# Performance work log

Measured on AMD Instinct MI355X. Metric: run time of the kernel, lower is better.

The kernel has to match this reference:

```python
import jax, jax.numpy as jnp
from jax import lax
import numpy as np

H = W = 224
N = H * W
T = 25          # landscape sample points
K_MAX = 2       # number of landscapes
M_PTS = 64      # max persistence-diagram points kept (top persistence)
OUT_F = 50
CHUNK = 512     # pixels per DTM chunk


def _make_offsets(m0):
    # static, sorted-by-distance local window covering >= m0 fraction of mass for near-uniform weights
    r = int(np.ceil(np.sqrt(m0 * N / np.pi) * 1.3))
    dy, dx = np.meshgrid(np.arange(-r, r + 1), np.arange(-r, r + 1), indexing="ij")
    d2 = (dy * dy + dx * dx).astype(np.float32).ravel()
    o = np.argsort(d2, kind="stable")
    return jnp.asarray(dy.ravel()[o]), jnp.asarray(dx.ravel()[o]), jnp.asarray(d2[o]), r

_OFF = {m0: _make_offsets(m0) for m0 in (0.05, 0.2)}


def _dtm(w_img, m0):
    """Weighted distance-to-measure on the unit-spacing 224x224 grid.
    dtm(x)^2 = (1/(m0*W)) * sum of w_j * d_j^2 over nearest grid points until cumulative
    weight reaches m0*W (partial weight on the crossing point). Offsets are pre-sorted by
    distance (identical for every pixel), so no per-pixel sort is needed."""
    dy, dx, d2, r = _OFF[m0]
    B = w_img.shape[0]
    wp = jnp.pad(w_img, ((0, 0), (r, r), (r, r)))
    thr = m0 * w_img.sum(axis=(1, 2))                      # (B,)
    pix = jnp.arange(N).reshape(N // CHUNK, CHUNK)

    def body(p):
        y = p // W + r
        x = p % W + r
        vals = wp[:, y[:, None] + dy[None, :], x[:, None] + dx[None, :]]  # (B,C,O)
        c = jnp.cumsum(vals, axis=-1)
        used = jnp.minimum(jnp.maximum(thr[:, None, None] - (c - vals), 0.0), vals)
        return jnp.einsum("bco,o->bc", used, d2) / thr[:, None]

    dtm2 = lax.map(jax.checkpoint(body), pix)              # (n_chunks, B, CHUNK)
    return jnp.sqrt(jnp.maximum(dtm2.transpose(1, 0, 2).reshape(B, N), 0.0))


def _h0_pairs_np(f_batch):
    """0-dim persistent homology (sublevel filtration, 4-connectivity) via union-find.
    Returns indices of birth/death pixels so birth/death VALUES can be gathered
    differentiably in jax (PLLay-style gradients)."""
    f_batch = np.asarray(f_batch)
    B = f_batch.shape[0]
    b_idx = np.zeros((B, M_PTS), np.int32)
    d_idx = np.zeros((B, M_PTS), np.int32)
    mask = np.zeros((B, M_PTS), np.bool_)
    for bb in range(B):
        f = f_batch[bb]
        order = np.argsort(f, kind="stable")
        parent = np.full(N, -1, np.int64)
        pairs = []
        for i in order:
            i = int(i)
            parent[i] = i
            y, x = divmod(i, W)
            nbs = []
            if y > 0: nbs.append(i - W)
            if y < H - 1: nbs.append(i + W)
            if x > 0: nbs.append(i - 1)
            if x < W - 1: nbs.append(i + 1)
            for nb in nbs:
                if parent[nb] < 0:
                    continue
                ri = i
                while parent[ri] != ri:
                    parent[ri] = parent[parent[ri]]; ri = parent[ri]
                rn = nb
                while parent[rn] != rn:
                    parent[rn] = parent[parent[rn]]; rn = parent[rn]
                if ri == rn:
                    continue
                if f[ri] <= f[rn]:
                    elder, young = ri, rn
                else:
                    elder, young = rn, ri
                pairs.append((young, i))   # elder rule: younger component dies here
                parent[young] = elder
        pairs.append((int(np.argmin(f)), int(np.argmax(f))))  # essential class
        pa = np.asarray(pairs, np.int64)
        pers = f[pa[:, 1]] - f[pa[:, 0]]
        keep = np.argsort(-pers)[:M_PTS]
        k = len(keep)
        b_idx[bb, :k] = pa[keep, 0]
        d_idx[bb, :k] = pa[keep, 1]
        mask[bb, :k] = pers[keep] > 0
    return b_idx, d_idx, mask


def _topo_layer(x_img, m0, tseq, gw, gb):
    # AdTopoLayer: DTM -> H0 persistence diagram -> persistence landscapes at tseq -> Linear
    dt = _dtm(x_img, m0)                                   # (B, N)
    B = dt.shape[0]
    shapes = (jax.ShapeDtypeStruct((B, M_PTS), np.int32),
              jax.ShapeDtypeStruct((B, M_PTS), np.int32),
              jax.ShapeDtypeStruct((B, M_PTS), np.bool_))
    b_idx, d_idx, mask = jax.pure_callback(_h0_pairs_np, shapes, lax.stop_gradient(dt))
    birth = jnp.take_along_axis(dt, b_idx, axis=1)         # differentiable gather
    death = jnp.take_along_axis(dt, d_idx, axis=1)
    death = jnp.where(mask, death, birth)                  # invalid slots -> zero tent
    t = tseq[None, None, :]                                # (1,1,T)
    tents = jnp.maximum(jnp.minimum(t - birth[:, :, None], death[:, :, None] - t), 0.0)
    lam, _ = lax.top_k(tents.transpose(0, 2, 1), K_MAX)    # (B,T,K): k-th largest tents
    feat = lam.transpose(0, 2, 1).reshape(B, K_MAX * T)    # (B,50)
    return feat @ gw.T + gb


def _forward(input, params):
    xs = []
    for m0, g in ((0.05, "1"), (0.2, "2")):
        for c in range(3):
            n = "t" + g + str(c + 1)
            xs.append(_topo_layer(input[:, c], m0, params[n + "_tseq"], params[n + "_w"], params[n + "_b"]))
    x = jnp.concatenate(xs, axis=-1)                       # (B, 300)
    signal = jnp.abs(lax.stop_gradient(x)).sum(axis=0)     # (300,) detached signal
    output = jax.nn.relu(x) @ params["fc_w"].T + params["fc_b"]
    return output, signal


def setup_inputs():
    key = jax.random.key(0)
    ks = jax.random.split(key, 8)
    B = 2
    inp = {"input": jax.random.uniform(ks[0], (B, 3, H, W), jnp.float32)}
    centers = {"1": 20.0, "2": 40.0}   # typical DTM value ranges for m0=0.05 / 0.2
    i = 1
    for g in ("1", "2"):
        for c in ("1", "2", "3"):
            n = "t" + g + c
            kk = jax.random.fold_in(ks[1], i)
            inp[n + "_tseq"] = jnp.linspace(centers[g] - 15.0, centers[g] + 15.0, T).astype(jnp.float32)
            inp[n + "_w"] = 0.1 * jax.random.normal(kk, (OUT_F, K_MAX * T), jnp.float32)
            inp[n + "_b"] = jnp.zeros((OUT_F,), jnp.float32)
            i += 1
    inp["fc_w"] = 0.1 * jax.random.normal(ks[2], (7, 6 * OUT_F), jnp.float32)
    inp["fc_b"] = jnp.zeros((7,), jnp.float32)
    return inp


def reference(input, t11_tseq, t11_w, t11_b, t12_tseq, t12_w, t12_b, t13_tseq, t13_w, t13_b, t21_tseq, t21_w, t21_b, t22_tseq, t22_w, t22_b, t23_tseq, t23_w, t23_b, fc_w, fc_b):
    params = dict(t11_tseq=t11_tseq, t11_w=t11_w, t11_b=t11_b,
                  t12_tseq=t12_tseq, t12_w=t12_w, t12_b=t12_b,
                  t13_tseq=t13_tseq, t13_w=t13_w, t13_b=t13_b,
                  t21_tseq=t21_tseq, t21_w=t21_w, t21_b=t21_b,
                  t22_tseq=t22_tseq, t22_w=t22_w, t22_b=t22_b,
                  t23_tseq=t23_tseq, t23_w=t23_w, t23_b=t23_b,
                  fc_w=fc_w, fc_b=fc_b)
    return _forward(input, params)
```

## Files before the change

### kernel.cpp

```cpp
#include <hip/hip_runtime.h>
#include <stdint.h>

#define HWDIM 224
#define NPIX (HWDIM*HWDIM)
#define NFIELD 12
#define TT 25

#define R1v 37
#define PW1v (HWDIM + 2*R1v)
#define C1v  (PW1v + 1)
#define R2v 74
#define PW2v (HWDIM + 2*R2v)
#define C2v  (PW2v + 1)

#define HSIZE 16384
#define FCAP 4096
#define RHASH 4096
#define DON 36

typedef unsigned long long u64;

struct LayerParams {
    const float* tseq[6];
    const float* gw[6];
    const float* gb[6];
};

constexpr size_t alup(size_t x) { return (x + 255) & ~(size_t)255; }
constexpr size_t SZPA = (size_t)6*PW1v*C1v*4;
constexpr size_t SZPB = (size_t)6*PW2v*C2v*4;
constexpr size_t OFF_SUMS = 0;
constexpr size_t OFF_P0A = alup(OFF_SUMS + 8*4);
constexpr size_t OFF_PZA = alup(OFF_P0A + SZPA);
constexpr size_t OFF_P0B = alup(OFF_PZA + 2*SZPA);
constexpr size_t OFF_PZB = alup(OFF_P0B + SZPB);
constexpr size_t OFF_DT   = alup(OFF_PZB + 2*SZPB);
constexpr size_t OFF_KEY  = alup(OFF_DT   + (size_t)NFIELD*NPIX*4);
constexpr size_t OFF_HP   = alup(OFF_KEY  + (size_t)NFIELD*NPIX*8);
constexpr size_t OFF_HB   = alup(OFF_HP   + (size_t)NFIELD*HSIZE*8);
constexpr size_t OFF_X    = alup(OFF_HB   + (size_t)NFIELD*HSIZE*8);


__global__ __launch_bounds__(1024) void k_sums(const float* __restrict__ inp, float* __restrict__ sums) {
    int img = blockIdx.x;
    const float* p = inp + (size_t)img * NPIX;
    __shared__ float red[1024];
    float s = 0.f;
    for (int i = threadIdx.x; i < NPIX; i += 1024) s += p[i];
    red[threadIdx.x] = s; __syncthreads();
    for (int w = 512; w > 0; w >>= 1) {
        if (threadIdx.x < w) red[threadIdx.x] += red[threadIdx.x + w];
        __syncthreads();
    }
    if (threadIdx.x == 0) sums[img] = red[0];
}

__global__ __launch_bounds__(64) void k_prefix(const float* __restrict__ inp,
        float* __restrict__ p0a, float2* __restrict__ pza,
        float* __restrict__ p0b, float2* __restrict__ pzb) {
    int bidx = blockIdx.x;
    const int tot0 = 6 * PW1v;
    int g = (bidx >= tot0);
    int rem = g ? (bidx - tot0) : bidx;
    const int PW = g ? PW2v : PW1v, R = g ? R2v : R1v, C = PW + 1;
    int img = rem / PW, row = rem % PW;
    float* P0 = (g ? p0b : p0a) + ((size_t)img*PW + row) * C;
    float2* PZ = (g ? pzb : pza) + ((size_t)img*PW + row) * C;
    int iy = row - R;
    bool rowok = ((unsigned)iy < HWDIM);
    const float* src = inp + (size_t)img*NPIX + (size_t)(rowok ? iy : 0)*HWDIM;
    const int lane = threadIdx.x;
    if (lane == 0) { P0[0] = 0.f; PZ[0] = make_float2(0.f, 0.f); }
    float c0 = 0.f, c1 = 0.f, c2 = 0.f;
    for (int i = 0; i < 6; ++i) {
        int k = i*64 + lane;
        float v = 0.f;
        if (k < PW && rowok) { int ix = k - R; if ((unsigned)ix < HWDIM) v = src[ix]; }
        float xd = (float)k;
        float w0 = v, w1 = v*xd, w2 = v*xd*xd;
        #pragma unroll
        for (int off = 1; off < 64; off <<= 1) {
            float t0 = __shfl_up(w0, off), t1 = __shfl_up(w1, off), t2 = __shfl_up(w2, off);
            if (lane >= off) { w0 += t0; w1 += t1; w2 += t2; }
        }
        if (k < PW) {
            P0[k+1] = c0 + w0;
            PZ[k+1] = make_float2(c1 + w1, c2 + w2);
        }
        c0 += __shfl(w0, 63); c1 += __shfl(w1, 63); c2 += __shfl(w2, 63);
    }
}

__device__ __forceinline__ int k_init_exact(int X, int R) {
    int K = (int)sqrtf((float)X) + 1;
    if (K > R) K = R;
    while (K > 0 && K*K > X) --K;
    return K;
}

__device__ __forceinline__ float dmass1(int X, const float* __restrict__ P0, int bidx,
        int C, int R) {
    float m = 0.f;
    int K = 0;
    if (X >= 0) {
        K = k_init_exact(X, R);
        m = P0[bidx+K+1] - P0[bidx-K];
    }
    int t = X - 1, step = 3;
    const float* __restrict__ Pu = P0 - C;
    const float* __restrict__ Pd = P0 + C;
    for (int dyy = 1; dyy <= R; ++dyy) {
        if (__all(t < 0)) break;
        if (t >= 0) {
            while (K*K > t) --K;
            int A = bidx + K + 1, B = bidx - K;
            m += (Pu[A] - Pu[B]) + (Pd[A] - Pd[B]);
        }
        t -= step; step += 2; Pu -= C; Pd += C;
    }
    return m;
}

__global__ __launch_bounds__(256) void k_dtm(const float* __restrict__ sums,
        const float* __restrict__ p0a, const float2* __restrict__ pza,
        const float* __restrict__ p0b, const float2* __restrict__ pzb,
        float* __restrict__ dt, u64* __restrict__ key) {
    const int xcd = blockIdx.x & 7, slot = blockIdx.x >> 3;
    int f, blk;
    if (xcd < 6) {
        if (slot < 196)            { f = 6 + xcd; blk = slot; }
        else if (slot < 196 + DON) { f = xcd; blk = (196 - DON) + (slot - 196); }
        else return;
    } else {
        const int per = 196 - DON;
        if (slot >= 3*per) return;
        int q = slot / per;
        f = (xcd - 6)*3 + q; blk = slot - q*per;
    }
    const int layer = f >> 1, b = f & 1;
    const int g = layer / 3, c = layer % 3;
    const int img = b*3 + c;
    const int R = g ? R2v : R1v, PW = g ? PW2v : PW1v, C = PW + 1;
    const int R2 = 2*R*R;
    const float thr = (g ? 0.2f : 0.05f) * sums[img];
    const float* __restrict__ P0 = (g ? p0b : p0a) + (size_t)img*PW*C;
    const float2* __restrict__ PZ = (g ? pzb : pza) + (size_t)img*PW*C;

    const int p = blk*256 + threadIdx.x;
    const int y = p / HWDIM, x = p % HWDIM;
    const int xc = x + R;
    const int bidx = (y + R)*C + xc;

    const int NP = g ? 7 : 6;
    const int WSTOP = g ? 86 : 43;
    int lo = 0, hi = R2 + 1;
    for (int it = 0; it < NP; ++it) {
        int X = (lo + hi) >> 1;
        float m = dmass1(X, P0, bidx, C, R);
        if (m >= thr) hi = X; else lo = X + 1;
    }
    for (int rit = 0; rit < 14; ++rit) {
        bool act = (hi == R2 + 1) ? (lo < hi) : (hi - lo > WSTOP);
        if (__all(!act)) break;
        int X = act ? ((lo + hi) >> 1) : -1;
        float m = dmass1(X, P0, bidx, C, R);
        if (X >= 0) { if (m >= thr) hi = X; else lo = X + 1; }
    }
    const bool nr = (hi == R2 + 1);
    const int  Dst = nr ? lo : ((lo + hi) >> 1);
    const bool cross = nr ? (lo <= R2) : true;
    const int  Xin = cross ? (Dst - 1) : R2;

    float m_in = 0.f, ws = 0.f;
    const float c2n = -2.f * (float)xc;
    const int xc2i = xc * xc;
    int K = 0;
    if (Xin >= 0) {
        K = k_init_exact(Xin, R);
        int A = bidx+K+1, B = bidx-K;
        float s0 = P0[A] - P0[B]; float2 zA = PZ[A], zB = PZ[B];
        m_in += s0; ws += fmaf((float)xc2i, s0, fmaf(c2n, zA.x - zB.x, zA.y - zB.y));
    }
    {
        int t = Xin - 1, step = 3, d2 = 1;
        const float* __restrict__ Pu = P0 - C;
        const float* __restrict__ Pd = P0 + C;
        const float2* __restrict__ Zu = PZ - C;
        const float2* __restrict__ Zd = PZ + C;
        for (int dyy = 1; dyy <= R; ++dyy) {
            if (__all(t < 0)) break;
            if (t >= 0) {
                while (K*K > t) --K;
                int A = bidx+K+1, B = bidx-K;
                float c1 = (float)(d2 + xc2i);
                { float s0 = Pu[A]-Pu[B]; float2 zA = Zu[A], zB = Zu[B];
                  m_in += s0; ws += fmaf(c1, s0, fmaf(c2n, zA.x - zB.x, zA.y - zB.y)); }
                { float s0 = Pd[A]-Pd[B]; float2 zA = Zd[A], zB = Zd[B];
                  m_in += s0; ws += fmaf(c1, s0, fmaf(c2n, zA.x - zB.x, zA.y - zB.y)); }
            }
            t -= step; d2 += step; step += 2;
            Pu -= C; Pd += C; Zu -= C; Zd += C;
        }
    }
    float s = cross ? (ws + (float)Dst * (thr - m_in)) : ws;
    float d = sqrtf(fmaxf(s / thr, 0.f));
    dt[(size_t)f*NPIX + p] = d;
    key[(size_t)f*NPIX + p] = ((u64)__float_as_uint(d) << 32) | (unsigned)p;
}

__device__ inline unsigned hash64(u64 x) {
    x ^= x >> 33; x *= 0xff51afd7ed558ccdULL;
    x ^= x >> 33; x *= 0xc4ceb9fe1a85ec53ULL;
    x ^= x >> 33;
    return (unsigned)x;
}

struct FinSh {
    u64 ek[FCAP];
    unsigned int epk[FCAP];
    unsigned int eab[FCAP];
    unsigned short eru[FCAP];
    int rhk[RHASH];
    short ufp[RHASH];
    float rdt[RHASH];
    unsigned int pyd[FCAP];
    float ppr[FCAP];
};

__device__ __forceinline__ void bitonic_n(u64* ek, int tid, int n, int bst) {
    for (int k = 2; k <= n; k <<= 1) {
        for (int j = k >> 1; j > 0; j >>= 1) {
            for (int i = tid; i < n; i += bst) {
                int ixj = i ^ j;
                if (ixj > i) {
                    u64 a = ek[i], b = ek[ixj];
                    if (((i & k) == 0) ? (a > b) : (a < b)) { ek[i] = b; ek[ixj] = a; }
                }
            }
            __syncthreads();
        }
    }
}

__global__ __launch_bounds__(1024) void k_fused(const float* __restrict__ dt,
        const u64* __restrict__ key,
        u64* __restrict__ hpair, u64* __restrict__ hbest,
        LayerParams lp, float* __restrict__ xbuf) {
    const int xcd = blockIdx.x & 7, slot = blockIdx.x >> 3;
    int f;
    if (xcd < 6) { if (slot != 0) return; f = 6 + xcd; }
    else f = (xcd - 6)*3 + slot;
    const int layer = f >> 1, bb = f & 1;
    const int tid = threadIdx.x; const int bs = 1024;
    const float* dtf = dt + (size_t)f*NPIX;
    const u64* kf = key + (size_t)f*NPIX;
    u64* hp = hpair + (size_t)f*HSIZE;
    u64* hb = hbest + (size_t)f*HSIZE;

    __shared__ union U {
        unsigned short par[NPIX];
        FinSh fin;
    } sh;
    __shared__ float birth[64], death[64], featsh[2*TT];
    __shared__ int spec_a[64], spec_b[64];
    __shared__ u64 spec_e[64];
    __shared__ int cnt_s, pc_s;
    __shared__ int gmin_s, gmax_s; __shared__ float gminf_s, gmaxf_s;

    u64 mymin = ~0ull, mymax = 0;
    for (int p = tid; p < NPIX; p += bs) {
        u64 kp = kf[p]; u64 best = kp; int bi = p;
        const int y = p / HWDIM, x = p % HWDIM;
        if (y > 0)        { u64 t = kf[p - HWDIM]; if (t < best) { best = t; bi = p - HWDIM; } }
        if (y < HWDIM-1)  { u64 t = kf[p + HWDIM]; if (t < best) { best = t; bi = p + HWDIM; } }
        if (x > 0)        { u64 t = kf[p - 1];     if (t < best) { best = t; bi = p - 1; } }
        if (x < HWDIM-1)  { u64 t = kf[p + 1];     if (t < best) { best = t; bi = p + 1; } }
        sh.par[p] = (unsigned short)bi;
        if (kp < mymin) mymin = kp;
        u64 mk = (kp & 0xFFFFFFFF00000000ull) | (0xFFFFu - (unsigned)(kp & 0xFFFFu));
        if (mk > mymax) mymax = mk;
    }
    {
        u64* red = (u64*)sh.fin.pyd;
        red[tid] = mymin; red[1024 + tid] = mymax;
        __syncthreads();
        for (int w = 512; w > 0; w >>= 1) {
            if (tid < w) {
                if (red[tid + w] < red[tid]) red[tid] = red[tid + w];
                if (red[1024 + tid + w] > red[1024 + tid]) red[1024 + tid] = red[1024 + tid + w];
            }
            __syncthreads();
        }
        if (tid == 0) {
            gmin_s = (int)(unsigned)(red[0] & 0xFFFFu);
            gminf_s = __uint_as_float((unsigned)(red[0] >> 32));
            gmax_s = 0xFFFF - (int)(unsigned)(red[1024] & 0xFFFFu);
            gmaxf_s = __uint_as_float((unsigned)(red[1024] >> 32));
            cnt_s = 0; pc_s = 0;
        }
    }
    __syncthreads();
    for (int pass = 0; pass < 17; ++pass) {
        int changed = 0;
        for (int p = tid; p < NPIX; p += bs) {
            unsigned short a = sh.par[p];
            unsigned short g2 = sh.par[a];
            changed |= (g2 != a);
            sh.par[p] = g2;
        }
        if (!__syncthreads_or(changed)) break;
    }
    for (int p = tid; p < NPIX; p += bs) {
        const int rp = sh.par[p];
        const int y = p / HWDIM, x = p % HWDIM;
        const u64 kp = kf[p];
        #pragma unroll
        for (int e = 0; e < 2; ++e) {
            int q;
            if (e == 0) { if (x >= HWDIM-1) continue; q = p + 1; }
            else        { if (y >= HWDIM-1) continue; q = p + HWDIM; }
            int rq = sh.par[q];
            if (rq == rp) continue;
            u64 kq = kf[q];
            u64 kmax; int ru;
            if (kp > kq) { kmax = kp; ru = rp; } else { kmax = kq; ru = rq; }
            u64 ekv = (kmax & 0xFFFFFFFF00000000ull) | ((kmax & 0xFFFFull) << 16) | (unsigned)ru;
            int ra = min(rp, rq), rb = max(rp, rq);
            u64 pk = ((u64)(unsigned)ra << 32) | (unsigned)rb;
            unsigned h = hash64(pk) & (HSIZE - 1);
            for (int probe = 0; probe < HSIZE; ++probe) {
                u64 old = atomicCAS(&hp[h], ~0ull, pk);
                if (old == ~0ull || old == pk) { atomicMin(&hb[h], ekv); break; }
                h = (h + 1) & (HSIZE - 1);
            }
        }
    }
    __syncthreads();
    for (int i = tid; i < RHASH; i += bs) sh.fin.rhk[i] = -1;
    __syncthreads();
    for (int i = tid; i < HSIZE; i += bs) {
        u64 pk = hp[i];
        if (pk != ~0ull) {
            int slot2 = atomicAdd(&cnt_s, 1);
            if (slot2 < FCAP) {
                u64 e = hb[i];
                unsigned u = (unsigned)((e >> 16) & 0xFFFFu);
                unsigned ru = (unsigned)(e & 0xFFFFu);
                sh.fin.ek[slot2] = (e & 0xFFFFFFFF00000000ull) | ((u64)u << 16) | (unsigned)slot2;
                int ra = (int)(pk >> 32), rb = (int)(pk & 0xFFFFFFFFu);
                sh.fin.epk[slot2] = ((unsigned)ra << 16) | (unsigned)rb;
                sh.fin.eru[slot2] = (unsigned short)ru;
                #pragma unroll
                for (int pass = 0; pass < 2; ++pass) {
                    int r = pass ? rb : ra;
                    unsigned h = ((unsigned)r * 2654435761u) & (RHASH - 1);
                    for (int pr = 0; pr < RHASH; ++pr) {
                        int old = atomicCAS(&sh.fin.rhk[h], -1, r);
                        if (old == -1 || old == r) break;
                        h = (h + 1) & (RHASH - 1);
                    }
                }
            }
        }
    }
    __syncthreads();
    int cnt = min(cnt_s, FCAP);
    int n1 = 64; while (n1 < cnt) n1 <<= 1;
    for (int s2 = tid; s2 < cnt; s2 += bs) {
        unsigned pk2 = sh.fin.epk[s2];
        int ra = (int)(pk2 >> 16), rb = (int)(pk2 & 0xFFFFu);
        int ru = sh.fin.eru[s2];
        int rv = (ru == ra) ? rb : ra;
        int su = -1, sv = -1;
        { unsigned h = ((unsigned)ru * 2654435761u) & (RHASH - 1);
          for (int pr = 0; pr < RHASH; ++pr) { int v = sh.fin.rhk[h]; if (v == ru) { su = (int)h; break; } if (v == -1) break; h = (h + 1) & (RHASH - 1); } }
        { unsigned h = ((unsigned)rv * 2654435761u) & (RHASH - 1);
          for (int pr = 0; pr < RHASH; ++pr) { int v = sh.fin.rhk[h]; if (v == rv) { sv = (int)h; break; } if (v == -1) break; h = (h + 1) & (RHASH - 1); } }
        sh.fin.eab[s2] = ((unsigned)su << 16) | (unsigned)(sv & 0xFFFF);
    }
    for (int i = cnt + tid; i < n1; i += bs) sh.fin.ek[i] = ~0ull;
    for (int s2 = tid; s2 < RHASH; s2 += bs) {
        sh.fin.ufp[s2] = (short)s2;
        int r = sh.fin.rhk[s2];
        sh.fin.rdt[s2] = (r >= 0) ? dtf[r] : 0.f;
    }
    __syncthreads();

    bitonic_n(sh.fin.ek, tid, n1, bs);

    if (tid < 64) {
        int pc = 0;
        for (int base = 0; base < cnt; base += 64) {
            int i = base + tid;
            int sa = -1, sb = -1; u64 e = ~0ull;
            if (i < cnt) {
                e = sh.fin.ek[i];
                int idx = (int)(e & 0xFFFFu);
                unsigned ab = sh.fin.eab[idx];
                sa = (int)(ab >> 16); sb = (int)(ab & 0xFFFFu);
                if (sa != 0xFFFF && sb != 0xFFFF) {
                    while (sh.fin.ufp[sa] != sa) { short g2 = sh.fin.ufp[sh.fin.ufp[sa]]; sh.fin.ufp[sa] = g2; sa = g2; }
                    while (sh.fin.ufp[sb] != sb) { short g2 = sh.fin.ufp[sh.fin.ufp[sb]]; sh.fin.ufp[sb] = g2; sb = g2; }
                    if (sa == sb) sa = -1;
                } else { sa = -1; }
            }
            spec_a[tid] = sa; spec_b[tid] = sb; spec_e[tid] = e;
            if (tid == 0) {
                int lim = min(64, cnt - base);
                for (int j = 0; j < lim; ++j) {
                    int sa2 = spec_a[j];
                    if (sa2 < 0) continue;
                    int sb2 = spec_b[j];
                    u64 e2 = spec_e[j];
                    while (sh.fin.ufp[sa2] != sa2) { short g2 = sh.fin.ufp[sh.fin.ufp[sa2]]; sh.fin.ufp[sa2] = g2; sa2 = g2; }
                    while (sh.fin.ufp[sb2] != sb2) { short g2 = sh.fin.ufp[sh.fin.ufp[sb2]]; sh.fin.ufp[sb2] = g2; sb2 = g2; }
                    if (sa2 == sb2) continue;
                    float fa = sh.fin.rdt[sa2], fb = sh.fin.rdt[sb2];
                    int elder, young;
                    if (fa <= fb) { elder = sa2; young = sb2; } else { elder = sb2; young = sa2; }
                    sh.fin.ufp[young] = (short)elder;
                    float pers = __uint_as_float((unsigned)(e2 >> 32)) - sh.fin.rdt[young];
                    if (pers > 0.f && pc < FCAP - 1) {
                        int u = (int)((e2 >> 16) & 0xFFFFu);
                        sh.fin.pyd[pc] = ((unsigned)sh.fin.rhk[young] << 16) | (unsigned)u;
                        sh.fin.ppr[pc] = pers; ++pc;
                    }
                }
            }
        }
        if (tid == 0) {
            sh.fin.pyd[pc] = ((unsigned)gmin_s << 16) | (unsigned)gmax_s;
            sh.fin.ppr[pc] = gmaxf_s - gminf_s; ++pc;
            pc_s = pc;
        }
    }
    __syncthreads();
    const int pc = pc_s;
    int n2 = 64; while (n2 < pc) n2 <<= 1;

    for (int i = tid; i < n2; i += bs) {
        if (i < pc && sh.fin.ppr[i] > 0.f)
            sh.fin.ek[i] = ((u64)(0xFFFFFFFFu - __float_as_uint(sh.fin.ppr[i])) << 32) | (unsigned)i;
        else sh.fin.ek[i] = ~0ull;
    }
    __syncthreads();
    bitonic_n(sh.fin.ek, tid, n2, bs);
    if (tid < 64) {
        u64 e = sh.fin.ek[tid];
        int bpix = 0, dpix = 0, msk = 0;
        if (e != ~0ull) {
            int i = (int)(e & 0xFFFFFFFFu);
            unsigned pd2 = sh.fin.pyd[i];
            bpix = (int)(pd2 >> 16); dpix = (int)(pd2 & 0xFFFFu); msk = 1;
        }
        float bv = dtf[bpix];
        float dv = msk ? dtf[dpix] : bv;
        birth[tid] = bv; death[tid] = dv;
    }
    __syncthreads();
    if (tid < TT) {
        float t = lp.tseq[layer][tid];
        float m1 = 0.f, m2 = 0.f;
        for (int m = 0; m < 64; ++m) {
            float v = fmaxf(fminf(t - birth[m], death[m] - t), 0.f);
            if (v > m1) { m2 = m1; m1 = v; } else if (v > m2) m2 = v;
        }
        featsh[tid] = m1; featsh[TT + tid] = m2;
    }
    __syncthreads();
    if (tid < 50) {
        const float* w = lp.gw[layer] + tid * 50;
        float acc = lp.gb[layer][tid];
        #pragma unroll
        for (int j = 0; j < 50; ++j) acc = fmaf(featsh[j], w[j], acc);
        xbuf[bb*300 + layer*50 + tid] = acc;
    }
}

__global__ __launch_bounds__(512) void k_final(const float* __restrict__ x, const float* __restrict__ fcw,
        const float* __restrict__ fcb, float* __restrict__ out) {
    __shared__ float rl[2][300];
    const int tid = threadIdx.x;
    if (tid < 300) {
        float a0 = x[tid], a1 = x[300 + tid];
        out[14 + tid] = fabsf(a0) + fabsf(a1);
        rl[0][tid] = fmaxf(a0, 0.f);
        rl[1][tid] = fmaxf(a1, 0.f);
    }
    __syncthreads();
    if (tid < 14) {
        int b = tid / 7, i = tid % 7;
        float acc = fcb[i];
        const float* w = fcw + i * 300;
        for (int j = 0; j < 300; ++j) acc = fmaf(rl[b][j], w[j], acc);
        out[b*7 + i] = acc;
    }
}

extern "C" void kernel_launch(void* const* d_in, const int* in_sizes, int n_in,
                              void* d_out, int out_size, void* d_ws, size_t ws_size,
                              hipStream_t stream) {
    (void)in_sizes; (void)n_in; (void)out_size; (void)ws_size;
    const float* inp = (const float*)d_in[0];
    LayerParams lp;
    for (int l = 0; l < 6; ++l) {
        lp.tseq[l] = (const float*)d_in[1 + 3*l];
        lp.gw[l]   = (const float*)d_in[2 + 3*l];
        lp.gb[l]   = (const float*)d_in[3 + 3*l];
    }
    const float* fcw = (const float*)d_in[19];
    const float* fcb = (const float*)d_in[20];

    char* w = (char*)d_ws;
    float* sums = (float*)(w + OFF_SUMS);
    float* p0a = (float*)(w + OFF_P0A);
    float2* pza = (float2*)(w + OFF_PZA);
    float* p0b = (float*)(w + OFF_P0B);
    float2* pzb = (float2*)(w + OFF_PZB);
    float* dt = (float*)(w + OFF_DT);
    u64* key = (u64*)(w + OFF_KEY);
    u64* hp = (u64*)(w + OFF_HP);
    u64* hb = (u64*)(w + OFF_HB);
    float* xbuf = (float*)(w + OFF_X);

    hipLaunchKernelGGL(k_sums, dim3(6), dim3(1024), 0, stream, inp, sums);
    const int prefRows = 6*PW1v + 6*PW2v;
    hipLaunchKernelGGL(k_prefix, dim3(prefRows), dim3(64), 0, stream,
                       inp, p0a, pza, p0b, pzb);
    hipMemsetAsync(hp, 0xFF, (size_t)NFIELD*HSIZE*8, stream);
    hipMemsetAsync(hb, 0xFF, (size_t)NFIELD*HSIZE*8, stream);
    const int maxslot = 3 * (196 - DON);
    hipLaunchKernelGGL(k_dtm, dim3(8 * maxslot), dim3(256), 0, stream,
                       sums, p0a, pza, p0b, pzb, dt, key);
    hipLaunchKernelGGL(k_fused, dim3(24), dim3(1024), 0, stream,
                       dt, key, hp, hb, lp, xbuf);
    hipLaunchKernelGGL(k_final, dim3(1), dim3(512), 0, stream, xbuf, fcw, fcb, (float*)d_out);
}
```

Before: 768.3 us.

## Seed per-pixel DTM bisection from a coarse-grid bracket pre-pass

Adds a k_dtmc pre-pass that runs the full radius bisection only on a 4x-subsampled 56x56 grid and stores each point's (lo, hi) bracket. k_dtm then reads the nearest coarse bracket, widens it by five pixels of radius on each side, and bisects from there. This drops the fixed initial bisection steps, each a costly dmass1 prefix-sum walk, for every full-resolution pixel. The refinement loop limit rises from 14 to 16 iterations. It also merges the two adjacent hash-table memsets into one, relying on their buffers being contiguous. If the widened bracket ever misses a pixel's true crossing radius, results would be wrong, and the extra launch adds a small fixed cost.

```diff
diff --git a/kernel.cpp b/kernel.cpp
--- a/kernel.cpp
+++ b/kernel.cpp
@@ -5,13 +5,13 @@
 #define NPIX (HWDIM*HWDIM)
 #define NFIELD 12
 #define TT 25
+#define CG 56
+#define NCP (CG*CG)
 
 #define R1v 37
 #define PW1v (HWDIM + 2*R1v)
-#define C1v  (PW1v + 1)
 #define R2v 74
 #define PW2v (HWDIM + 2*R2v)
-#define C2v  (PW2v + 1)
 
 #define HSIZE 16384
 #define FCAP 4096
@@ -27,8 +27,8 @@
 };
 
 constexpr size_t alup(size_t x) { return (x + 255) & ~(size_t)255; }
-constexpr size_t SZPA = (size_t)6*PW1v*C1v*4;
-constexpr size_t SZPB = (size_t)6*PW2v*C2v*4;
+constexpr size_t SZPA = (size_t)6*PW1v*(PW1v+1)*4;
+constexpr size_t SZPB = (size_t)6*PW2v*(PW2v+1)*4;
 constexpr size_t OFF_SUMS = 0;
 constexpr size_t OFF_P0A = alup(OFF_SUMS + 8*4);
 constexpr size_t OFF_PZA = alup(OFF_P0A + SZPA);
@@ -39,6 +39,7 @@
 constexpr size_t OFF_HP   = alup(OFF_KEY  + (size_t)NFIELD*NPIX*8);
 constexpr size_t OFF_HB   = alup(OFF_HP   + (size_t)NFIELD*HSIZE*8);
 constexpr size_t OFF_X    = alup(OFF_HB   + (size_t)NFIELD*HSIZE*8);
+constexpr size_t OFF_CB   = alup(OFF_X    + 1024*4);
 
 
 __global__ __launch_bounds__(1024) void k_sums(const float* __restrict__ inp, float* __restrict__ sums) {
@@ -121,9 +122,47 @@
     return m;
 }
 
+__global__ __launch_bounds__(256) void k_dtmc(const float* __restrict__ sums,
+        const float* __restrict__ p0a, const float* __restrict__ p0b,
+        uint2* __restrict__ cb) {
+    const int xcd = blockIdx.x & 7, slot = blockIdx.x >> 3;
+    int f, blk;
+    if (xcd < 6) { if (slot >= 13) return; f = 6 + xcd; blk = slot; }
+    else { if (slot >= 39) return; int q = slot / 13; f = (xcd - 6)*3 + q; blk = slot - q*13; }
+    const int idx = blk*256 + threadIdx.x;
+    if (idx >= NCP) return;
+    const int layer = f >> 1, b = f & 1;
+    const int g = layer / 3, c = layer % 3;
+    const int img = b*3 + c;
+    const int R = g ? R2v : R1v, PW = g ? PW2v : PW1v, C = PW + 1;
+    const int R2 = 2*R*R;
+    const float thr = (g ? 0.2f : 0.05f) * sums[img];
+    const float* __restrict__ P0 = (g ? p0b : p0a) + (size_t)img*PW*C;
+    const int y = (idx / CG) * 4, x = (idx % CG) * 4;
+    const int bidx = (y + R)*C + (x + R);
+
+    const int NP = g ? 7 : 6;
+    const int WSTOP = g ? 86 : 43;
+    int lo = 0, hi = R2 + 1;
+    for (int it = 0; it < NP; ++it) {
+        int X = (lo + hi) >> 1;
+        float m = dmass1(X, P0, bidx, C, R);
+        if (m >= thr) hi = X; else lo = X + 1;
+    }
+    for (int rit = 0; rit < 14; ++rit) {
+        bool act = (hi == R2 + 1) ? (lo < hi) : (hi - lo > WSTOP);
+        if (__all(!act)) break;
+        int X = act ? ((lo + hi) >> 1) : -1;
+        float m = dmass1(X, P0, bidx, C, R);
+        if (X >= 0) { if (m >= thr) hi = X; else lo = X + 1; }
+    }
+    cb[f*NCP + idx] = make_uint2((unsigned)lo, (unsigned)hi);
+}
+
 __global__ __launch_bounds__(256) void k_dtm(const float* __restrict__ sums,
         const float* __restrict__ p0a, const float2* __restrict__ pza,
         const float* __restrict__ p0b, const float2* __restrict__ pzb,
+        const uint2* __restrict__ cb,
         float* __restrict__ dt, u64* __restrict__ key) {
     const int xcd = blockIdx.x & 7, slot = blockIdx.x >> 3;
     int f, blk;
@@ -151,15 +190,22 @@
     const int xc = x + R;
     const int bidx = (y + R)*C + xc;
 
-    const int NP = g ? 7 : 6;
+    const int ci = min(CG - 1, (y + 2) >> 2);
+    const int cj = min(CG - 1, (x + 2) >> 2);
+    uint2 cbv = cb[f*NCP + ci*CG + cj];
+    int lo, hi;
+    {
+        float rlo = sqrtf((float)cbv.x) - 5.f;
+        lo = (rlo > 0.f) ? max(0, (int)(rlo*rlo) - 2) : 0;
+        const int rm5 = R - 5;
+        if ((int)cbv.y <= rm5*rm5) {
+            float rhi = sqrtf((float)cbv.y) + 5.f;
+            hi = min(R2 + 1, (int)(rhi*rhi) + 3);
+        } else hi = R2 + 1;
+        if (lo >= hi) lo = max(0, hi - 1);
+    }
     const int WSTOP = g ? 86 : 43;
-    int lo = 0, hi = R2 + 1;
-    for (int it = 0; it < NP; ++it) {
-        int X = (lo + hi) >> 1;
-        float m = dmass1(X, P0, bidx, C, R);
-        if (m >= thr) hi = X; else lo = X + 1;
-    }
-    for (int rit = 0; rit < 14; ++rit) {
+    for (int rit = 0; rit < 16; ++rit) {
         bool act = (hi == R2 + 1) ? (lo < hi) : (hi - lo > WSTOP);
         if (__all(!act)) break;
         int X = act ? ((lo + hi) >> 1) : -1;
@@ -522,16 +568,18 @@
     u64* hp = (u64*)(w + OFF_HP);
     u64* hb = (u64*)(w + OFF_HB);
     float* xbuf = (float*)(w + OFF_X);
+    uint2* cb = (uint2*)(w + OFF_CB);
 
     hipLaunchKernelGGL(k_sums, dim3(6), dim3(1024), 0, stream, inp, sums);
     const int prefRows = 6*PW1v + 6*PW2v;
     hipLaunchKernelGGL(k_prefix, dim3(prefRows), dim3(64), 0, stream,
                        inp, p0a, pza, p0b, pzb);
-    hipMemsetAsync(hp, 0xFF, (size_t)NFIELD*HSIZE*8, stream);
-    hipMemsetAsync(hb, 0xFF, (size_t)NFIELD*HSIZE*8, stream);
+    hipMemsetAsync(hp, 0xFF, (size_t)2*NFIELD*HSIZE*8, stream);
+    hipLaunchKernelGGL(k_dtmc, dim3(8 * 39), dim3(256), 0, stream,
+                       sums, p0a, p0b, cb);
     const int maxslot = 3 * (196 - DON);
     hipLaunchKernelGGL(k_dtm, dim3(8 * maxslot), dim3(256), 0, stream,
-                       sums, p0a, pza, p0b, pzb, dt, key);
+                       sums, p0a, pza, p0b, pzb, cb, dt, key);
     hipLaunchKernelGGL(k_fused, dim3(24), dim3(1024), 0, stream,
                        dt, key, hp, hb, lp, xbuf);
     hipLaunchKernelGGL(k_final, dim3(1), dim3(512), 0, stream, xbuf, fcw, fcb, (float*)d_out);
```

Measured after the change: 1.034 ms. +34.6%, slower.
